# Kernel optimization log

Hardware: AMD Instinct MI355X
Metric: run time of the kernel (lower is better)

## Reference

```python
import jax, jax.numpy as jnp
import numpy as np

N = 100000
E = 1600000
F_IN = 128
H1 = 256
H2 = 192  # HIDDEN_LAYER_SIZE - 64
C = 32


def _sage_conv(x, src, dst, W_l, W_r, b):
    # PyG SAGEConv (mean aggr): out = mean_{j in N(i)} x_j @ W_l + x_i @ W_r + b
    n = x.shape[0]
    summed = jax.ops.segment_sum(x[src], dst, num_segments=n)   # [N, d]
    cnt = jax.ops.segment_sum(jnp.ones((src.shape[0],), x.dtype), dst, num_segments=n)
    mean = summed / jnp.maximum(cnt, 1.0)[:, None]
    return mean @ W_l + x @ W_r + b


def setup_inputs() -> dict:
    key = jax.random.key(0)
    ks = jax.random.split(key, 10)
    x = jax.random.normal(ks[0], (N, F_IN), dtype=jnp.float32)
    edge_index = jax.random.randint(ks[1], (2, E), 0, N, dtype=jnp.int64)
    def glorot(k, fan_in, fan_out):
        s = jnp.sqrt(2.0 / (fan_in + fan_out)).astype(jnp.float32)
        return jax.random.normal(k, (fan_in, fan_out), dtype=jnp.float32) * s
    return {
        "x": x,
        "edge_index": edge_index,
        "W1_l": glorot(ks[2], F_IN, H1), "W1_r": glorot(ks[3], F_IN, H1), "b1": jnp.zeros((H1,), jnp.float32),
        "W2_l": glorot(ks[4], H1, H2), "W2_r": glorot(ks[5], H1, H2), "b2": jnp.zeros((H2,), jnp.float32),
        "W3_l": glorot(ks[6], H2, C), "W3_r": glorot(ks[7], H2, C), "b3": jnp.zeros((C,), jnp.float32),
    }


def reference(x, edge_index, W1_l, W1_r, b1, W2_l, W2_r, b2, W3_l, W3_r, b3):
    src, dst = edge_index[0], edge_index[1]
    h = jnp.tanh(_sage_conv(x, src, dst, W1_l, W1_r, b1))
    h = jax.nn.relu(_sage_conv(h, src, dst, W2_l, W2_r, b2))
    h = _sage_conv(h, src, dst, W3_l, W3_r, b3)
    return jax.nn.sigmoid(h)
```

## Files before the change

kernel.cpp:

```cpp
#include <hip/hip_runtime.h>
#include <hip/hip_fp16.h>
#include <math.h>

typedef unsigned short u16;
typedef unsigned int u32;
typedef unsigned char u8;
typedef __attribute__((ext_vector_type(8))) short bf16x8;
typedef __attribute__((ext_vector_type(4))) float f32x4;

static inline int idiv(int a, int b) { return (a + b - 1) / b; }

__device__ inline float b2f_lo(u32 w) { return __uint_as_float((w & 0xFFFFu) << 16); }
__device__ inline float b2f_hi(u32 w) { return __uint_as_float(w & 0xFFFF0000u); }
__device__ inline u32 f2b_rne(float f) {
    u32 x = __float_as_uint(f);
    return (x + 0x7FFFu + ((x >> 16) & 1u)) >> 16;
}

#if defined(__has_builtin)
#if __has_builtin(__builtin_amdgcn_cvt_pk_f32_fp8) && __has_builtin(__builtin_amdgcn_cvt_pk_fp8_f32)
#define FP8_HW 1
#endif
#endif

__device__ inline float fp8_dec1_sw(u32 b) {
    u32 s = (b & 0x80u) << 24;
    u32 em = b & 0x7Fu;
    if (em >= 8u) {
        u32 e = em >> 3, m = em & 7u;
        return __uint_as_float(s | ((e + 120u) << 23) | (m << 20));
    }
    float v = (float)(int)em * 0.001953125f;
    return (b & 0x80u) ? -v : v;
}
__device__ inline u32 fp8_enc1_sw(float f) {
    __half hh = __float2half(f * 0.00390625f);
    u16 hb = __half_as_ushort(hh);
    u32 mag = hb & 0x7FFFu;
    u32 rm = (mag + 0x3Fu + ((mag >> 7) & 1u)) >> 7;
    if (rm > 0x7Eu) rm = 0x7Eu;
    return ((hb >> 8) & 0x80u) | rm;
}

__device__ inline void fp8x4_dec(u32 w, float o[4]) {
#ifdef FP8_HW
    auto lo = __builtin_amdgcn_cvt_pk_f32_fp8((int)w, false);
    auto hi = __builtin_amdgcn_cvt_pk_f32_fp8((int)w, true);
    o[0] = lo[0]; o[1] = lo[1]; o[2] = hi[0]; o[3] = hi[1];
#else
    o[0] = fp8_dec1_sw(w & 0xFFu); o[1] = fp8_dec1_sw((w >> 8) & 0xFFu);
    o[2] = fp8_dec1_sw((w >> 16) & 0xFFu); o[3] = fp8_dec1_sw(w >> 24);
#endif
}
__device__ inline void fp8x2_dec(u32 w, float o[2]) {
#ifdef FP8_HW
    auto lo = __builtin_amdgcn_cvt_pk_f32_fp8((int)w, false);
    o[0] = lo[0]; o[1] = lo[1];
#else
    o[0] = fp8_dec1_sw(w & 0xFFu); o[1] = fp8_dec1_sw((w >> 8) & 0xFFu);
#endif
}
__device__ inline u32 fp8x4_enc(float a, float b, float c, float d) {
#ifdef FP8_HW
    int p = __builtin_amdgcn_cvt_pk_fp8_f32(a, b, 0, false);
    p = __builtin_amdgcn_cvt_pk_fp8_f32(c, d, p, true);
    return (u32)p;
#else
    return fp8_enc1_sw(a) | (fp8_enc1_sw(b) << 8) | (fp8_enc1_sw(c) << 16) | (fp8_enc1_sw(d) << 24);
#endif
}

__device__ __forceinline__ void g2lds16(const u16* gsrc, u16* ldsbase) {
    __builtin_amdgcn_global_load_lds(
        (const __attribute__((address_space(1))) u32*)gsrc,
        (__attribute__((address_space(3))) u32*)ldsbase, 16, 0, 0);
}


#define SCAP 14336

__global__ void part_kernel(const int* __restrict__ src, const int* __restrict__ dst,
                            int E, int n, int cap,
                            int* __restrict__ pcur, uint2* __restrict__ ebuf) {
    __shared__ int lcnt[128], lbase[128], lpos[128];
    const int nb = gridDim.x;
    const int e0 = (int)((long long)E * blockIdx.x / nb);
    const int e1 = (int)((long long)E * (blockIdx.x + 1) / nb);
    if (threadIdx.x < 128) { lcnt[threadIdx.x] = 0; lpos[threadIdx.x] = 0; }
    __syncthreads();
    for (int e = e0 + (int)threadIdx.x; e < e1; e += 256) {
        int d = dst[e];
        if ((unsigned)d >= (unsigned)n) continue;
        int g = (int)((long long)d * 128 / n);
        atomicAdd(&lcnt[g], 1);
    }
    __syncthreads();
    if (threadIdx.x < 128)
        lbase[threadIdx.x] = atomicAdd(&pcur[threadIdx.x], lcnt[threadIdx.x]);
    __syncthreads();
    for (int e = e0 + (int)threadIdx.x; e < e1; e += 256) {
        int d = dst[e];
        if ((unsigned)d >= (unsigned)n) continue;
        int s = src[e];
        int g = (int)((long long)d * 128 / n);
        int off = lbase[g] + atomicAdd(&lpos[g], 1);
        if (off < cap) ebuf[(size_t)g * cap + off] = make_uint2((u32)d, (u32)s);
    }
}

__global__ void subscan_kernel(const int* __restrict__ pcur, int* __restrict__ subbase,
                               int* __restrict__ rp, int n, int cap) {
    __shared__ int s[128];
    int v = pcur[threadIdx.x]; if (v > cap) v = cap;
    s[threadIdx.x] = v;
    __syncthreads();
    for (int off = 1; off < 128; off <<= 1) {
        int t = ((int)threadIdx.x >= off) ? s[threadIdx.x - off] : 0;
        __syncthreads();
        s[threadIdx.x] += t;
        __syncthreads();
    }
    subbase[threadIdx.x] = s[threadIdx.x] - v;
    if (threadIdx.x == 127) rp[n] = s[127];
}

__global__ __launch_bounds__(1024)
void fill3_kernel(const uint2* __restrict__ ebuf, const int* __restrict__ pcur,
                  const int* __restrict__ subbase, int cap, int n,
                  int* __restrict__ rp, float* __restrict__ dinv, int* __restrict__ col) {
    __shared__ u32 stage[SCAP];
    __shared__ int lcnt[800];
    __shared__ int lscan[1024];
    __shared__ int s_ned;
    const int g = blockIdx.x;
    const int lo = (int)(((long long)g * n + 127) / 128);
    const int hi = (int)(((long long)(g + 1) * n + 127) / 128);
    const int nn = hi - lo;
    const int t = threadIdx.x;
    int pc = pcur[g]; if (pc > cap) pc = cap;
    const uint2* base_e = ebuf + (size_t)g * cap;

    if (t < 800) lcnt[t] = 0;
    __syncthreads();
    for (int e = t; e < pc; e += 1024) {
        int idx = (int)base_e[e].x - lo;
        if ((unsigned)idx < (unsigned)nn) atomicAdd(&lcnt[idx], 1);
    }
    __syncthreads();
    int v = (t < nn) ? lcnt[t] : 0;
    lscan[t] = v;
    __syncthreads();
    for (int off = 1; off < 1024; off <<= 1) {
        int tv = (t >= off) ? lscan[t - off] : 0;
        __syncthreads();
        lscan[t] += tv;
        __syncthreads();
    }
    const int gbase = subbase[g];
    const int excl = lscan[t] - v;
    if (t < nn) {
        rp[lo + t]   = gbase + excl;
        dinv[lo + t] = 1.0f / (float)(v > 1 ? v : 1);
        lcnt[t] = excl;
    }
    if (t == 1023) s_ned = lscan[1023];
    __syncthreads();
    const int ned = s_ned;
    const bool ovf = ned > SCAP;
    for (int e = t; e < pc; e += 1024) {
        uint2 r = base_e[e];
        int idx = (int)r.x - lo;
        if ((unsigned)idx < (unsigned)nn) {
            int s = (int)r.y;
            if ((unsigned)s >= (unsigned)n) s = 0;
            int pos = atomicAdd(&lcnt[idx], 1);
            if (!ovf) stage[pos] = (u32)s;
            else col[gbase + pos] = s;
        }
    }
    __syncthreads();
    if (!ovf)
        for (int k = t; k < ned; k += 1024) col[gbase + k] = (int)stage[k];
}

__global__ void prep_all(const float* __restrict__ W1l, const float* __restrict__ W1r,
                         const float* __restrict__ W2l, const float* __restrict__ W2r,
                         const float* __restrict__ W3l, const float* __restrict__ W3r,
                         const float* __restrict__ b2, const float* __restrict__ b3,
                         u16* __restrict__ W1lt, u16* __restrict__ W1rt,
                         u16* __restrict__ W2t, u16* __restrict__ W3t,
                         float* __restrict__ b2cat, float* __restrict__ b3cat) {
    int i = blockIdx.x * 256 + threadIdx.x;
    if (i < 32768) {
        int nn = i >> 7, k = i & 127;
        W1lt[i] = (u16)f2b_rne(W1l[k * 256 + nn]);
        return;
    }
    i -= 32768;
    if (i < 32768) {
        int nn = i >> 7, k = i & 127;
        W1rt[i] = (u16)f2b_rne(W1r[k * 256 + nn]);
        return;
    }
    i -= 32768;
    if (i < 49152) {
        int nn = i >> 8, k = i & 255;
        W2t[i] = (u16)f2b_rne(W2l[k * 192 + nn]);
        return;
    }
    i -= 49152;
    if (i < 49152) {
        int nn = i >> 8, k = i & 255;
        W2t[192 * 256 + i] = (u16)f2b_rne(W2r[k * 192 + nn]);
        return;
    }
    i -= 49152;
    if (i < 6144) {
        int nn = i / 192, k = i - nn * 192;
        W3t[i] = (u16)f2b_rne(W3l[k * 32 + nn]);
        return;
    }
    i -= 6144;
    if (i < 6144) {
        int nn = i / 192, k = i - nn * 192;
        W3t[32 * 192 + i] = (u16)f2b_rne(W3r[k * 32 + nn]);
        return;
    }
    i -= 6144;
    if (i < 384) { b2cat[i] = (i < 192) ? 0.f : b2[i - 192]; return; }
    i -= 384;
    if (i < 64)  { b3cat[i] = (i < 32) ? 0.f : b3[i - 32]; }
}

__global__ void cvt_x_kernel(const float* __restrict__ x, u16* __restrict__ xb,
                             u8* __restrict__ xq, int total8) {
    int i = blockIdx.x * 256 + threadIdx.x;
    if (i >= total8) return;
    const float4 a = *(const float4*)(x + (size_t)i * 8);
    const float4 b = *(const float4*)(x + (size_t)i * 8 + 4);
    uint4 o;
    o.x = f2b_rne(a.x) | (f2b_rne(a.y) << 16);
    o.y = f2b_rne(a.z) | (f2b_rne(a.w) << 16);
    o.z = f2b_rne(b.x) | (f2b_rne(b.y) << 16);
    o.w = f2b_rne(b.z) | (f2b_rne(b.w) << 16);
    *(uint4*)(xb + (size_t)i * 8) = o;
    uint2 q;
    q.x = fp8x4_enc(a.x, a.y, a.z, a.w);
    q.y = fp8x4_enc(b.x, b.y, b.z, b.w);
    *(uint2*)(xq + (size_t)i * 8) = q;
}


__global__ void agg_mean128(const u8* __restrict__ Xq, const int* __restrict__ rp,
                            const int* __restrict__ col, const float* __restrict__ dinv,
                            u16* __restrict__ A, int n, int E) {
    const int widx = (blockIdx.x * blockDim.x + threadIdx.x) >> 6;
    const int lane = threadIdx.x & 63;
    const int half = lane >> 5, sl = lane & 31;
    const int node = widx * 2 + half;
    const bool valid = node < n;
    const int s   = valid ? rp[node] : 0;
    const int deg = valid ? rp[node + 1] - s : 0;
    int m = deg;
    m = max(m, __shfl_xor(m, 32));
    const u32* Xg = (const u32*)Xq;
    float a[4] = {0, 0, 0, 0}, c[4] = {0, 0, 0, 0};
    for (int t = 0; t < m; t += 4) {
        bool p0 = t < deg, p1 = t + 1 < deg, p2 = t + 2 < deg, p3 = t + 3 < deg;
        int i0 = min(s + t,     E - 1), i1 = min(s + t + 1, E - 1);
        int i2 = min(s + t + 2, E - 1), i3 = min(s + t + 3, E - 1);
        int e0 = col[i0], e1 = col[i1], e2 = col[i2], e3 = col[i3];
        u32 w0 = Xg[(size_t)e0 * 32 + sl];
        u32 w1 = Xg[(size_t)e1 * 32 + sl];
        u32 w2 = Xg[(size_t)e2 * 32 + sl];
        u32 w3 = Xg[(size_t)e3 * 32 + sl];
        if (!p0) w0 = 0;
        if (!p1) w1 = 0;
        if (!p2) w2 = 0;
        if (!p3) w3 = 0;
        float d0[4], d1[4], d2[4], d3[4];
        fp8x4_dec(w0, d0); fp8x4_dec(w1, d1); fp8x4_dec(w2, d2); fp8x4_dec(w3, d3);
#pragma unroll
        for (int jj = 0; jj < 4; ++jj) { a[jj] += d0[jj] + d2[jj]; c[jj] += d1[jj] + d3[jj]; }
    }
    if (valid) {
        const float inv = dinv[node];
        uint2 o;
        o.x = f2b_rne((a[0] + c[0]) * inv) | (f2b_rne((a[1] + c[1]) * inv) << 16);
        o.y = f2b_rne((a[2] + c[2]) * inv) | (f2b_rne((a[3] + c[3]) * inv) << 16);
        *((uint2*)A + (size_t)node * 32 + sl) = o;
    }
}

__global__ void agg_cat192(const u8* __restrict__ Yq, const u16* __restrict__ Yr,
                           const int* __restrict__ rp, const int* __restrict__ col,
                           const float* __restrict__ dinv, u16* __restrict__ H,
                           int n, int E) {
    const int widx = (blockIdx.x * blockDim.x + threadIdx.x) >> 6;
    const int lane = threadIdx.x & 63;
    const int half = lane >> 5, sl = lane & 31;
    const int node = widx * 2 + half;
    const bool valid = node < n;
    const int s   = valid ? rp[node] : 0;
    const int deg = valid ? rp[node + 1] - s : 0;
    int m = deg;
    m = max(m, __shfl_xor(m, 32));
    const int offd = 4 * sl, offs = 128 + 2 * sl;
    float a[6] = {0, 0, 0, 0, 0, 0};
    float b[6] = {0, 0, 0, 0, 0, 0};
    float c[6] = {0, 0, 0, 0, 0, 0};
    for (int t = 0; t < m; t += 3) {
        bool p0 = t < deg, p1 = t + 1 < deg, p2 = t + 2 < deg;
        int i0 = min(s + t, E - 1), i1 = min(s + t + 1, E - 1), i2 = min(s + t + 2, E - 1);
        int e0 = col[i0], e1 = col[i1], e2 = col[i2];
        const u8* r0 = Yq + (size_t)e0 * 192;
        const u8* r1 = Yq + (size_t)e1 * 192;
        const u8* r2 = Yq + (size_t)e2 * 192;
        u32 w0 = *(const u32*)(r0 + offd);
        u32 w1 = *(const u32*)(r1 + offd);
        u32 w2 = *(const u32*)(r2 + offd);
        u32 s0 = *(const u16*)(r0 + offs);
        u32 s1 = *(const u16*)(r1 + offs);
        u32 s2 = *(const u16*)(r2 + offs);
        if (!p0) { w0 = 0; s0 = 0; }
        if (!p1) { w1 = 0; s1 = 0; }
        if (!p2) { w2 = 0; s2 = 0; }
        float d[4], e2f[2];
        fp8x4_dec(w0, d); fp8x2_dec(s0, e2f);
        a[0] += d[0]; a[1] += d[1]; a[2] += d[2]; a[3] += d[3];
        a[4] += e2f[0]; a[5] += e2f[1];
        fp8x4_dec(w1, d); fp8x2_dec(s1, e2f);
        b[0] += d[0]; b[1] += d[1]; b[2] += d[2]; b[3] += d[3];
        b[4] += e2f[0]; b[5] += e2f[1];
        fp8x4_dec(w2, d); fp8x2_dec(s2, e2f);
        c[0] += d[0]; c[1] += d[1]; c[2] += d[2]; c[3] += d[3];
        c[4] += e2f[0]; c[5] += e2f[1];
    }
    if (valid) {
        const float inv = dinv[node];
        const char* rs = (const char*)Yr + (size_t)node * 384;
        uint2 ru = *(const uint2*)(rs + 8 * sl);
        u32   rd = *(const u32*)(rs + 256 + 4 * sl);
        float o0 = fmaxf((a[0] + b[0] + c[0]) * inv + b2f_lo(ru.x), 0.f);
        float o1 = fmaxf((a[1] + b[1] + c[1]) * inv + b2f_hi(ru.x), 0.f);
        float o2 = fmaxf((a[2] + b[2] + c[2]) * inv + b2f_lo(ru.y), 0.f);
        float o3 = fmaxf((a[3] + b[3] + c[3]) * inv + b2f_hi(ru.y), 0.f);
        float o4 = fmaxf((a[4] + b[4] + c[4]) * inv + b2f_lo(rd), 0.f);
        float o5 = fmaxf((a[5] + b[5] + c[5]) * inv + b2f_hi(rd), 0.f);
        char* hb = (char*)H + (size_t)node * 384;
        uint2 ou; ou.x = f2b_rne(o0) | (f2b_rne(o1) << 16);
        ou.y = f2b_rne(o2) | (f2b_rne(o3) << 16);
        *(uint2*)(hb + 8 * sl) = ou;
        *(u32*)(hb + 256 + 4 * sl) = f2b_rne(o4) | (f2b_rne(o5) << 16);
    }
}

__global__ void agg_cat32(const u16* __restrict__ Y, const int* __restrict__ rp,
                          const int* __restrict__ col, const float* __restrict__ dinv,
                          float* __restrict__ out, int n, int E) {
    const int widx = (blockIdx.x * blockDim.x + threadIdx.x) >> 6;
    const int lane = threadIdx.x & 63;
    const int grp = lane >> 4, sl = lane & 15;
    const int node = widx * 4 + grp;
    const bool valid = node < n;
    const int s   = valid ? rp[node] : 0;
    const int deg = valid ? rp[node + 1] - s : 0;
    int m = deg;
    m = max(m, __shfl_xor(m, 16));
    m = max(m, __shfl_xor(m, 32));
    const u32* Yw = (const u32*)Y;
    float a0 = 0, a1 = 0, b0 = 0, b1 = 0;
    for (int t = 0; t < m; t += 4) {
        bool p0 = t < deg, p1 = t + 1 < deg, p2 = t + 2 < deg, p3 = t + 3 < deg;
        int i0 = min(s + t,     E - 1), i1 = min(s + t + 1, E - 1);
        int i2 = min(s + t + 2, E - 1), i3 = min(s + t + 3, E - 1);
        int e0 = col[i0], e1 = col[i1], e2 = col[i2], e3 = col[i3];
        u32 w0 = Yw[(size_t)e0 * 32 + sl];
        u32 w1 = Yw[(size_t)e1 * 32 + sl];
        u32 w2 = Yw[(size_t)e2 * 32 + sl];
        u32 w3 = Yw[(size_t)e3 * 32 + sl];
        if (!p0) w0 = 0;
        if (!p1) w1 = 0;
        if (!p2) w2 = 0;
        if (!p3) w3 = 0;
        a0 += b2f_lo(w0); a1 += b2f_hi(w0);
        b0 += b2f_lo(w1); b1 += b2f_hi(w1);
        a0 += b2f_lo(w2); a1 += b2f_hi(w2);
        b0 += b2f_lo(w3); b1 += b2f_hi(w3);
    }
    if (valid) {
        const float inv = dinv[node];
        u32 rv = Yw[(size_t)node * 32 + 16 + sl];
        float o0 = 1.f / (1.f + __expf(-((a0 + b0) * inv + b2f_lo(rv))));
        float o1 = 1.f / (1.f + __expf(-((a1 + b1) * inv + b2f_hi(rv))));
        *(float2*)(out + (size_t)node * 32 + sl * 2) = make_float2(o0, o1);
    }
}

template <int KDIM, int NDIM, int BN, int ACT, bool DUAL, bool SPLITQ>
__global__ __launch_bounds__(256)
void gemm_mfma(const u16* __restrict__ A1, const u16* __restrict__ A2,
               const u16* __restrict__ B1t, const u16* __restrict__ B2t,
               const float* __restrict__ bias, u16* __restrict__ out,
               u8* __restrict__ outq, int M) {
    constexpr int BM = 128;
    constexpr int WR = (BN == 128) ? 2 : 4;
    constexpr int MF = BM / WR / 16;
    constexpr int NF = 4;
    constexpr int BNP = BN + 8;
    constexpr int SMEM = (BM * 64 + BN * 64 > BM * BNP) ? (BM * 64 + BN * 64) : (BM * BNP);
    __shared__ u16 smem[SMEM];
    u16* As = smem;
    u16* Bs = smem + BM * 64;
    u16* tile = smem;

    const int row0 = blockIdx.x * BM;
    const int bn0  = blockIdx.y * BN;
    const int t    = threadIdx.x;
    const int wid  = t >> 6, ln = t & 63;
    const int lr   = ln >> 3;
    const int lc   = ln & 7;
    const int ln15 = ln & 15, lg = ln >> 4;
    const int wr = (BN == 128) ? (wid >> 1) : wid;
    const int wc = (BN == 128) ? (wid & 1) : 0;
    const int wrow0 = wr * (BM / WR);
    const int wcol0 = wc * 64;
    const int swch  = (lc ^ lr) * 8;

    f32x4 acc[MF][NF];
#pragma unroll
    for (int m = 0; m < MF; ++m)
#pragma unroll
        for (int nn = 0; nn < NF; ++nn) acc[m][nn] = (f32x4){0.f, 0.f, 0.f, 0.f};

#pragma unroll
    for (int s = 0; s < (DUAL ? 2 : 1); ++s) {
        const u16* A  = (DUAL && s) ? A2 : A1;
        const u16* Bt = (DUAL && s) ? B2t : B1t;
        for (int kt = 0; kt < KDIM / 64; ++kt) {
            const int k0 = kt * 64;
#pragma unroll
            for (int it = 0; it < 4; ++it) {
                int rloc = it * 32 + 8 * wid + lr;
                int grow = row0 + rloc; if (grow >= M) grow = M - 1;
                g2lds16(A + (size_t)grow * KDIM + k0 + swch,
                        As + (it * 32 + 8 * wid) * 64);
            }
#pragma unroll
            for (int it = 0; it < BN / 32; ++it) {
                int rloc = it * 32 + 8 * wid + lr;
                g2lds16(Bt + (size_t)(bn0 + rloc) * KDIM + k0 + swch,
                        Bs + (it * 32 + 8 * wid) * 64);
            }
            __syncthreads();
#pragma unroll
            for (int ks = 0; ks < 2; ++ks) {
                bf16x8 af[MF], bfr[NF];
#pragma unroll
                for (int m = 0; m < MF; ++m) {
                    int r  = wrow0 + m * 16 + ln15;
                    int ch = (ks * 4 + lg) ^ (r & 7);
                    af[m] = *(const bf16x8*)(As + r * 64 + ch * 8);
                }
#pragma unroll
                for (int nn = 0; nn < NF; ++nn) {
                    int r  = wcol0 + nn * 16 + ln15;
                    int ch = (ks * 4 + lg) ^ (r & 7);
                    bfr[nn] = *(const bf16x8*)(Bs + r * 64 + ch * 8);
                }
#pragma unroll
                for (int m = 0; m < MF; ++m)
#pragma unroll
                    for (int nn = 0; nn < NF; ++nn)
                        acc[m][nn] = __builtin_amdgcn_mfma_f32_16x16x32_bf16(
                            af[m], bfr[nn], acc[m][nn], 0, 0, 0);
            }
            __syncthreads();
        }
    }

#pragma unroll
    for (int nn = 0; nn < NF; ++nn) {
        const int colt = wcol0 + nn * 16 + ln15;
        const float bv = bias[bn0 + colt];
#pragma unroll
        for (int m = 0; m < MF; ++m) {
#pragma unroll
            for (int r = 0; r < 4; ++r) {
                const int rowt = wrow0 + m * 16 + lg * 4 + r;
                float v = acc[m][nn][r] + bv;
                if (ACT == 0) v = tanhf(v);
                tile[rowt * BNP + colt] = (u16)f2b_rne(v);
            }
        }
    }
    __syncthreads();

#pragma unroll
    for (int it = 0; it < BM * BN / (8 * 256); ++it) {
        const int idx  = it * 256 + t;
        const int rowt = idx / (BN / 8);
        const int cv   = idx % (BN / 8);
        const int grow = row0 + rowt;
        if (grow < M) {
            uint4 v = *(const uint4*)(tile + rowt * BNP + cv * 8);
            if (SPLITQ) {
                const int gcol = bn0 + cv * 8;
                if (gcol < 192) {
                    uint2 q;
                    q.x = fp8x4_enc(b2f_lo(v.x), b2f_hi(v.x), b2f_lo(v.y), b2f_hi(v.y));
                    q.y = fp8x4_enc(b2f_lo(v.z), b2f_hi(v.z), b2f_lo(v.w), b2f_hi(v.w));
                    *(uint2*)(outq + (size_t)grow * 192 + gcol) = q;
                } else {
                    *(uint4*)(out + (size_t)grow * 192 + (gcol - 192)) = v;
                }
            } else {
                *(uint4*)(out + (size_t)grow * NDIM + bn0 + cv * 8) = v;
            }
        }
    }
}


extern "C" void kernel_launch(void* const* d_in, const int* in_sizes, int n_in,
                              void* d_out, int out_size, void* d_ws, size_t ws_size,
                              hipStream_t stream) {
    const float* x   = (const float*)d_in[0];
    const int*   ei  = (const int*)  d_in[1];
    const float* W1l = (const float*)d_in[2];
    const float* W1r = (const float*)d_in[3];
    const float* b1  = (const float*)d_in[4];
    const float* W2l = (const float*)d_in[5];
    const float* W2r = (const float*)d_in[6];
    const float* b2  = (const float*)d_in[7];
    const float* W3l = (const float*)d_in[8];
    const float* W3r = (const float*)d_in[9];
    const float* b3  = (const float*)d_in[10];
    float* out = (float*)d_out;

    const int n = in_sizes[0] / 128;
    const int E = in_sizes[1] / 2;
    const int* esrc = ei;
    const int* edst = ei + E;

    char* ws = (char*)d_ws;
    size_t off = 0;
    auto alloc = [&](size_t bytes) -> void* {
        void* p = ws + off;
        off += (bytes + 255) & ~(size_t)255;
        return p;
    };
    int*   rp     = (int*)  alloc((size_t)(n + 1) * 4);
    int*   colx   = (int*)  alloc((size_t)E * 4);
    float* dinv   = (float*)alloc((size_t)n * 4);
    int*   pcur   = (int*)  alloc(128 * 4);
    int*   subbase= (int*)  alloc(128 * 4);
    u16*   W1lt  = (u16*)  alloc(256 * 128 * 2);
    u16*   W1rt  = (u16*)  alloc(256 * 128 * 2);
    u16*   W2t   = (u16*)  alloc(384 * 256 * 2);
    u16*   W3t   = (u16*)  alloc(64 * 192 * 2);
    float* b2cat = (float*)alloc(384 * 4);
    float* b3cat = (float*)alloc(64 * 4);
    u16*   Sa    = (u16*)  alloc((size_t)n * 384 * 2);
    u16*   Sb    = (u16*)  alloc((size_t)n * 256 * 2);

    if (off > ws_size) return;

    u16* xb   = Sa;
    u16* AGG1 = Sa + (size_t)n * 128;
    u8*  xq   = (u8*)(Sa + (size_t)n * 256);
    u16* Y2r  = Sa;
    u8*  Y2q  = (u8*)(Sa + (size_t)n * 192);
    u16* Y3   = Sa;
    uint2* ebuf = (uint2*)Sb;
    u16* H1   = Sb;
    u16* H2   = Sb;

    const int GX = idiv(n, 128);
    const int cap = SCAP;

    hipMemsetAsync(pcur, 0, 128 * 4, stream);
    part_kernel<<<512, 256, 0, stream>>>(esrc, edst, E, n, cap, pcur, ebuf);
    subscan_kernel<<<1, 128, 0, stream>>>(pcur, subbase, rp, n, cap);
    fill3_kernel<<<128, 1024, 0, stream>>>(ebuf, pcur, subbase, cap, n, rp, dinv, colx);

    prep_all<<<idiv(176576, 256), 256, 0, stream>>>(
        W1l, W1r, W2l, W2r, W3l, W3r, b2, b3, W1lt, W1rt, W2t, W3t, b2cat, b3cat);
    cvt_x_kernel<<<idiv(n * 16, 256), 256, 0, stream>>>(x, xb, xq, n * 16);

    agg_mean128<<<idiv(n, 8), 256, 0, stream>>>(xq, rp, colx, dinv, AGG1, n, E);
    gemm_mfma<128, 256, 128, 0, true, false><<<dim3(GX, 2), 256, 0, stream>>>(
        AGG1, xb, W1lt, W1rt, b1, H1, (u8*)nullptr, n);

    gemm_mfma<256, 384, 128, -1, false, true><<<dim3(GX, 3), 256, 0, stream>>>(
        H1, (const u16*)nullptr, W2t, (const u16*)nullptr, b2cat, Y2r, Y2q, n);
    agg_cat192<<<idiv(n, 8), 256, 0, stream>>>(Y2q, Y2r, rp, colx, dinv, H2, n, E);

    gemm_mfma<192, 64, 64, -1, false, false><<<dim3(GX, 1), 256, 0, stream>>>(
        H2, (const u16*)nullptr, W3t, (const u16*)nullptr, b3cat, Y3, (u8*)nullptr, n);
    agg_cat32<<<idiv(n, 16), 256, 0, stream>>>(Y3, rp, colx, dinv, out, n, E);
}
```

Measured before the change: 303.3 us.

## Double-buffer LDS tiles in MFMA GEMM to overlap loads with compute

Converts the GEMM main loop to a two-stage LDS pipeline: the next K-tile is fetched via global_load_lds into the alternate buffer while MFMAs run on the current one, with an explicit vmcnt wait plus barrier per step. It flattens the dual-operand loop into one unrolled tile sequence. This is meant to hide global load latency behind compute, at the cost of doubling LDS usage, which may reduce occupancy.

```diff
diff --git a/kernel.cpp b/kernel.cpp
--- a/kernel.cpp
+++ b/kernel.cpp
@@ -74,6 +74,12 @@
     __builtin_amdgcn_global_load_lds(
         (const __attribute__((address_space(1))) u32*)gsrc,
         (__attribute__((address_space(3))) u32*)ldsbase, 16, 0, 0);
+}
+
+__device__ __forceinline__ void pipe_barrier() {
+    asm volatile("s_waitcnt vmcnt(0)" ::: "memory");
+    __builtin_amdgcn_s_barrier();
+    asm volatile("" ::: "memory");
 }
 
 
@@ -408,10 +414,11 @@
     constexpr int MF = BM / WR / 16;
     constexpr int NF = 4;
     constexpr int BNP = BN + 8;
-    constexpr int SMEM = (BM * 64 + BN * 64 > BM * BNP) ? (BM * 64 + BN * 64) : (BM * BNP);
+    constexpr int BUF = BM * 64 + BN * 64;
+    constexpr int SMEM = (2 * BUF > BM * BNP) ? (2 * BUF) : (BM * BNP);
+    constexpr int NT = KDIM / 64;
+    constexpr int T  = (DUAL ? 2 : 1) * NT;
     __shared__ u16 smem[SMEM];
-    u16* As = smem;
-    u16* Bs = smem + BM * 64;
     u16* tile = smem;
 
     const int row0 = blockIdx.x * BM;
@@ -433,26 +440,49 @@
 #pragma unroll
         for (int nn = 0; nn < NF; ++nn) acc[m][nn] = (f32x4){0.f, 0.f, 0.f, 0.f};
 
-#pragma unroll
-    for (int s = 0; s < (DUAL ? 2 : 1); ++s) {
-        const u16* A  = (DUAL && s) ? A2 : A1;
-        const u16* Bt = (DUAL && s) ? B2t : B1t;
-        for (int kt = 0; kt < KDIM / 64; ++kt) {
-            const int k0 = kt * 64;
+    {
+        const u16* A  = A1;
+        const u16* Bt = B1t;
+        u16* As = smem;
+        u16* Bs = smem + BM * 64;
+#pragma unroll
+        for (int it = 0; it < 4; ++it) {
+            int rloc = it * 32 + 8 * wid + lr;
+            int grow = row0 + rloc; if (grow >= M) grow = M - 1;
+            g2lds16(A + (size_t)grow * KDIM + swch, As + (it * 32 + 8 * wid) * 64);
+        }
+#pragma unroll
+        for (int it = 0; it < BN / 32; ++it) {
+            int rloc = it * 32 + 8 * wid + lr;
+            g2lds16(Bt + (size_t)(bn0 + rloc) * KDIM + swch, Bs + (it * 32 + 8 * wid) * 64);
+        }
+    }
+    pipe_barrier();
+
+#pragma unroll
+    for (int tt = 0; tt < T; ++tt) {
+        if (tt + 1 < T) {
+            const int tn = tt + 1;
+            const u16* A  = (DUAL && tn >= NT) ? A2 : A1;
+            const u16* Bt = (DUAL && tn >= NT) ? B2t : B1t;
+            const int k0 = ((tn >= NT) ? (tn - NT) : tn) * 64;
+            u16* As = smem + (tn & 1) * BUF;
+            u16* Bs = As + BM * 64;
 #pragma unroll
             for (int it = 0; it < 4; ++it) {
                 int rloc = it * 32 + 8 * wid + lr;
                 int grow = row0 + rloc; if (grow >= M) grow = M - 1;
-                g2lds16(A + (size_t)grow * KDIM + k0 + swch,
-                        As + (it * 32 + 8 * wid) * 64);
+                g2lds16(A + (size_t)grow * KDIM + k0 + swch, As + (it * 32 + 8 * wid) * 64);
             }
 #pragma unroll
             for (int it = 0; it < BN / 32; ++it) {
                 int rloc = it * 32 + 8 * wid + lr;
-                g2lds16(Bt + (size_t)(bn0 + rloc) * KDIM + k0 + swch,
-                        Bs + (it * 32 + 8 * wid) * 64);
+                g2lds16(Bt + (size_t)(bn0 + rloc) * KDIM + k0 + swch, Bs + (it * 32 + 8 * wid) * 64);
             }
-            __syncthreads();
+        }
+        {
+            const u16* As = smem + (tt & 1) * BUF;
+            const u16* Bs = As + BM * 64;
 #pragma unroll
             for (int ks = 0; ks < 2; ++ks) {
                 bf16x8 af[MF], bfr[NF];
@@ -475,9 +505,10 @@
                         acc[m][nn] = __builtin_amdgcn_mfma_f32_16x16x32_bf16(
                             af[m], bfr[nn], acc[m][nn], 0, 0, 0);
             }
-            __syncthreads();
         }
-    }
+        pipe_barrier();
+    }
+    __syncthreads();
 
 #pragma unroll
     for (int nn = 0; nn < NF; ++nn) {
```

Measured after the change: 316.8 us. +4.4%, slower.
